# Kernel optimization log

Measured on AMD Instinct MI355X. Metric: run time of the kernel, lower is better.

## Reference

```python
import jax, jax.numpy as jnp
import numpy as np

ATTN_SIZE = 64
ENC_SIZE = 512
HIDDEN_SIZE = 512
L, B = 2048, 64


def setup_inputs() -> dict:
    key = jax.random.key(0)
    k1, k2, k3, k4, k5, k6 = jax.random.split(key, 6)
    enc_outputs = jax.random.normal(k1, (L, B, ENC_SIZE), dtype=jnp.float32)
    lens = jax.random.randint(k2, (B,), 1, L + 1, dtype=jnp.int32)
    hidden_states = jax.random.normal(k3, (B, HIDDEN_SIZE), dtype=jnp.float32)
    # Xavier-normal params as in reset_params()
    W_enc = jax.random.normal(k4, (ENC_SIZE, ATTN_SIZE), dtype=jnp.float32) * np.sqrt(2.0 / (ENC_SIZE + ATTN_SIZE))
    W_hidden = jax.random.normal(k5, (HIDDEN_SIZE, ATTN_SIZE), dtype=jnp.float32) * np.sqrt(2.0 / (HIDDEN_SIZE + ATTN_SIZE))
    b_attn = jnp.zeros((ATTN_SIZE,), dtype=jnp.float32)
    v = jax.random.normal(k6, (ATTN_SIZE,), dtype=jnp.float32)
    return {"enc_outputs": enc_outputs, "lens": lens, "hidden_states": hidden_states,
            "W_enc": W_enc, "b_attn": b_attn, "W_hidden": W_hidden, "v": v}


def reference(enc_outputs, lens, hidden_states, W_enc, b_attn, W_hidden, v):
    l = enc_outputs.shape[0]
    # parts: (l, b, attn_size) — projection of encoder outputs
    parts = jnp.einsum('lbd,da->lba', enc_outputs, W_enc) + b_attn
    # additive (Bahdanau) score: tanh(parts + h @ W_hidden) . v -> (l, b)
    hid = hidden_states @ W_hidden  # (b, attn_size)
    scores = jnp.sum(jnp.tanh(parts + hid[None, :, :]) * v, axis=2)
    # faithful mask: 1.0 at valid positions, -inf at padding (original adds 1, a
    # constant shift that softmax cancels, but we reproduce the exact math)
    valid = jnp.arange(l, dtype=lens.dtype)[:, None] < lens[None, :]  # (l, b)
    mask = jnp.where(valid, jnp.float32(1.0), -jnp.inf)
    w = jax.nn.softmax(scores + mask, axis=0)  # softmax over sequence dim
    # weighted sum over sequence: (b, d)
    return jnp.einsum('lb,lbd->bd', w, enc_outputs)
```

## Files before the change

kernel.cpp:

```cpp
#include <hip/hip_runtime.h>
#include <hip/hip_bf16.h>
#include <math.h>

#define L_DIM 2048
#define B_DIM 64
#define D_DIM 512
#define A_DIM 64

#define CHUNK_L 64
#define SUB_L 32
#define N_CHUNK (L_DIM / CHUNK_L)
#define EPAD 520

typedef __attribute__((ext_vector_type(8))) short bf16x8;
typedef __attribute__((ext_vector_type(4))) float f32x4;

__device__ __forceinline__ void split_bf16(float x, short& hi, short& lo) {
    __hip_bfloat16 h = __float2bfloat16(x);
    float hf = __bfloat162float(h);
    __hip_bfloat16 l = __float2bfloat16(x - hf);
    hi = *reinterpret_cast<short*>(&h);
    lo = *reinterpret_cast<short*>(&l);
}
__device__ __forceinline__ float bf16s_to_f(short s) {
    unsigned int u = ((unsigned int)(unsigned short)s) << 16;
    return __uint_as_float(u);
}

__global__ void hb_kernel(const float* __restrict__ hidden,
                          const float* __restrict__ Wh,
                          const float* __restrict__ battn,
                          float* __restrict__ hb) {
    const int b = blockIdx.x;
    const int a = threadIdx.x;
    const float* hrow = hidden + b * D_DIM;
    float acc = battn[a];
#pragma unroll 8
    for (int d = 0; d < D_DIM; ++d) acc += hrow[d] * Wh[d * A_DIM + a];
    hb[b * A_DIM + a] = acc;
}

__global__ __launch_bounds__(256) void wt_kernel(const float* __restrict__ We,
                                                 short* __restrict__ wt_hi,
                                                 short* __restrict__ wt_lo) {
    const int idx = blockIdx.x * 256 + threadIdx.x;
    const int a = idx & 63;
    const int d = idx >> 6;
    float x = We[d * A_DIM + a];
    short h, l;
    split_bf16(x, h, l);
    wt_hi[a * D_DIM + d] = h;
    wt_lo[a * D_DIM + d] = l;
}

__global__ __launch_bounds__(256) void fused_kernel(
    const float* __restrict__ enc, const short* __restrict__ wt_hi,
    const short* __restrict__ wt_lo, const float* __restrict__ hb,
    const float* __restrict__ v, const int* __restrict__ lens,
    float* __restrict__ Om, float* __restrict__ mz) {
    const int c = blockIdx.x;
    const int b = blockIdx.y;
    const int tid = threadIdx.x;
    const int wave = tid >> 6;
    const int lane = tid & 63;
    const int quad = lane >> 4;
    const int l15 = lane & 15;

    __shared__ short Ehi[SUB_L][EPAD];
    __shared__ short Elo[SUB_L][EPAD];
    __shared__ float sred[SUB_L][2];
    __shared__ float wl[SUB_L];
    __shared__ float red[4][D_DIM];
    __shared__ float msc[2];

    const int len_b = lens[b];

    const int lt = wave >> 1;
    const int ah = wave & 1;
    const int a0 = (2 * ah) * 16 + l15;
    const int a1 = a0 + 16;

    const float hb0 = hb[b * A_DIM + a0];
    const float hb1 = hb[b * A_DIM + a1];
    const float v0 = v[a0];
    const float v1 = v[a1];

    float Oacc[8];
#pragma unroll
    for (int i = 0; i < 8; ++i) Oacc[i] = 0.f;
    float mA = -INFINITY, ZA = 0.f;

    const int g = tid >> 6;
    const int d0 = (tid & 63) * 8;

#pragma unroll 1
    for (int sub = 0; sub < 2; ++sub) {
        const int l_base = c * CHUNK_L + sub * SUB_L;

        __syncthreads();

        {
            const float* src = enc + ((size_t)l_base * B_DIM + b) * D_DIM;
#pragma unroll
            for (int j = 0; j < 16; ++j) {
                const int idx = tid + 256 * j;
                const int li = idx >> 7;
                const int po = idx & 127;
                const float4 x =
                    *(const float4*)(src + (size_t)li * B_DIM * D_DIM + po * 4);
                short4 h4, l4;
                split_bf16(x.x, h4.x, l4.x);
                split_bf16(x.y, h4.y, l4.y);
                split_bf16(x.z, h4.z, l4.z);
                split_bf16(x.w, h4.w, l4.w);
                *(short4*)&Ehi[li][po * 4] = h4;
                *(short4*)&Elo[li][po * 4] = l4;
            }
        }
        __syncthreads();

        f32x4 acc0 = {0.f, 0.f, 0.f, 0.f};
        f32x4 acc1 = {0.f, 0.f, 0.f, 0.f};
        const short* brow0h = wt_hi + (size_t)a0 * D_DIM + quad * 8;
        const short* brow0l = wt_lo + (size_t)a0 * D_DIM + quad * 8;
        const short* brow1h = wt_hi + (size_t)a1 * D_DIM + quad * 8;
        const short* brow1l = wt_lo + (size_t)a1 * D_DIM + quad * 8;
        const int arow = lt * 16 + l15;
#pragma unroll 4
        for (int s = 0; s < 16; ++s) {
            const int k = s * 32;
            const bf16x8 Ah = *(const bf16x8*)&Ehi[arow][k + quad * 8];
            const bf16x8 Al = *(const bf16x8*)&Elo[arow][k + quad * 8];
            const bf16x8 B0h = *(const bf16x8*)(brow0h + k);
            const bf16x8 B0l = *(const bf16x8*)(brow0l + k);
            const bf16x8 B1h = *(const bf16x8*)(brow1h + k);
            const bf16x8 B1l = *(const bf16x8*)(brow1l + k);
            acc0 = __builtin_amdgcn_mfma_f32_16x16x32_bf16(Ah, B0h, acc0, 0, 0, 0);
            acc0 = __builtin_amdgcn_mfma_f32_16x16x32_bf16(Ah, B0l, acc0, 0, 0, 0);
            acc0 = __builtin_amdgcn_mfma_f32_16x16x32_bf16(Al, B0h, acc0, 0, 0, 0);
            acc1 = __builtin_amdgcn_mfma_f32_16x16x32_bf16(Ah, B1h, acc1, 0, 0, 0);
            acc1 = __builtin_amdgcn_mfma_f32_16x16x32_bf16(Ah, B1l, acc1, 0, 0, 0);
            acc1 = __builtin_amdgcn_mfma_f32_16x16x32_bf16(Al, B1h, acc1, 0, 0, 0);
        }

#pragma unroll
        for (int r = 0; r < 4; ++r) {
            float t = tanhf(acc0[r] + hb0) * v0 + tanhf(acc1[r] + hb1) * v1;
            t += __shfl_xor(t, 1);
            t += __shfl_xor(t, 2);
            t += __shfl_xor(t, 4);
            t += __shfl_xor(t, 8);
            if (l15 == 0) sred[lt * 16 + quad * 4 + r][ah] = t;
        }
        __syncthreads();

        if (tid < 32) {
            const int lg = l_base + tid;
            float s = sred[tid][0] + sred[tid][1];
            s = (lg < len_b) ? (s + 1.0f) : -INFINITY;
            float m = s;
            m = fmaxf(m, __shfl_xor(m, 1));
            m = fmaxf(m, __shfl_xor(m, 2));
            m = fmaxf(m, __shfl_xor(m, 4));
            m = fmaxf(m, __shfl_xor(m, 8));
            m = fmaxf(m, __shfl_xor(m, 16));
            const float w = (m == -INFINITY) ? 0.f : expf(s - m);
            wl[tid] = w;
            float z = w;
            z += __shfl_xor(z, 1);
            z += __shfl_xor(z, 2);
            z += __shfl_xor(z, 4);
            z += __shfl_xor(z, 8);
            z += __shfl_xor(z, 16);
            if (tid == 0) { msc[0] = m; msc[1] = z; }
        }
        __syncthreads();

        float pa[8];
#pragma unroll
        for (int i = 0; i < 8; ++i) pa[i] = 0.f;
#pragma unroll
        for (int li = 0; li < 8; ++li) {
            const int l = g * 8 + li;
            const float w = wl[l];
            const bf16x8 h8 = *(const bf16x8*)&Ehi[l][d0];
            const bf16x8 l8 = *(const bf16x8*)&Elo[l][d0];
#pragma unroll
            for (int i = 0; i < 8; ++i) {
                pa[i] += w * (bf16s_to_f(h8[i]) + bf16s_to_f(l8[i]));
            }
        }
        *(float4*)&red[g][d0] = make_float4(pa[0], pa[1], pa[2], pa[3]);
        *(float4*)&red[g][d0 + 4] = make_float4(pa[4], pa[5], pa[6], pa[7]);
        __syncthreads();

        const float m_sub = msc[0], Z_sub = msc[1];
        const float mN = fmaxf(mA, m_sub);
        const float cA = (mA == -INFINITY) ? 0.f : expf(mA - mN);
        const float cS = (m_sub == -INFINITY) ? 0.f : expf(m_sub - mN);
        if (tid < 64) {
            const int dd = tid * 8;
#pragma unroll
            for (int i = 0; i < 8; ++i) {
                const float os =
                    red[0][dd + i] + red[1][dd + i] + red[2][dd + i] + red[3][dd + i];
                Oacc[i] = cA * Oacc[i] + cS * os;
            }
        }
        ZA = cA * ZA + cS * Z_sub;
        mA = mN;
    }

    if (tid < 64) {
        float* dst = Om + ((size_t)b * N_CHUNK + c) * D_DIM + tid * 8;
        *(float4*)dst = make_float4(Oacc[0], Oacc[1], Oacc[2], Oacc[3]);
        *(float4*)(dst + 4) = make_float4(Oacc[4], Oacc[5], Oacc[6], Oacc[7]);
    }
    if (tid == 0) {
        mz[((size_t)b * N_CHUNK + c) * 2 + 0] = mA;
        mz[((size_t)b * N_CHUNK + c) * 2 + 1] = ZA;
    }
}

__global__ __launch_bounds__(256) void combine_kernel(
    const float* __restrict__ Om, const float* __restrict__ mz,
    float* __restrict__ out) {
    const int b = blockIdx.x;
    const int tid = threadIdx.x;
    __shared__ float coef[N_CHUNK];
    __shared__ float sinv;

    if (tid < 32) {
        const float m = mz[((size_t)b * N_CHUNK + tid) * 2 + 0];
        const float Z = mz[((size_t)b * N_CHUNK + tid) * 2 + 1];
        float mm = m;
        mm = fmaxf(mm, __shfl_xor(mm, 1));
        mm = fmaxf(mm, __shfl_xor(mm, 2));
        mm = fmaxf(mm, __shfl_xor(mm, 4));
        mm = fmaxf(mm, __shfl_xor(mm, 8));
        mm = fmaxf(mm, __shfl_xor(mm, 16));
        const float cc = (m == -INFINITY) ? 0.f : expf(m - mm);
        coef[tid] = cc;
        float s = cc * Z;
        s += __shfl_xor(s, 1);
        s += __shfl_xor(s, 2);
        s += __shfl_xor(s, 4);
        s += __shfl_xor(s, 8);
        s += __shfl_xor(s, 16);
        if (tid == 0) sinv = 1.0f / s;
    }
    __syncthreads();

    const float* base = Om + (size_t)b * N_CHUNK * D_DIM + tid * 2;
    float ox = 0.f, oy = 0.f;
#pragma unroll 8
    for (int cc = 0; cc < N_CHUNK; ++cc) {
        const float2 x = *(const float2*)(base + cc * D_DIM);
        ox += coef[cc] * x.x;
        oy += coef[cc] * x.y;
    }
    const float s = sinv;
    *(float2*)(out + (size_t)b * D_DIM + tid * 2) = make_float2(ox * s, oy * s);
}

__global__ __launch_bounds__(256) void scores_kernel(
    const float* __restrict__ enc, const float* __restrict__ We,
    const float* __restrict__ hb, const float* __restrict__ v,
    const int* __restrict__ lens, float* __restrict__ scores) {
    const int l = blockIdx.x;
    const int tid = threadIdx.x;
    const int ty = tid >> 4;
    const int tx = tid & 15;

    __shared__ float As[32][68];
    __shared__ float Bs[32][68];
    __shared__ float redl[64][17];

    float acc[4][4] = {};
    float4 areg[2], breg[2];
    const float* encl = enc + (size_t)l * B_DIM * D_DIM;

    auto loadTiles = [&](int k0) {
#pragma unroll
        for (int i = 0; i < 2; ++i) {
            const int cc = tid + 256 * i;
            const int bb = cc >> 3, kq = cc & 7;
            areg[i] = *(const float4*)(encl + bb * D_DIM + k0 + kq * 4);
            const int kk = cc >> 4, a4 = (cc & 15) * 4;
            breg[i] = *(const float4*)(We + (k0 + kk) * A_DIM + a4);
        }
    };
    auto storeTiles = [&]() {
#pragma unroll
        for (int i = 0; i < 2; ++i) {
            const int cc = tid + 256 * i;
            const int bb = cc >> 3, kq = cc & 7;
            As[kq * 4 + 0][bb] = areg[i].x;
            As[kq * 4 + 1][bb] = areg[i].y;
            As[kq * 4 + 2][bb] = areg[i].z;
            As[kq * 4 + 3][bb] = areg[i].w;
            const int kk = cc >> 4, a4 = (cc & 15) * 4;
            *(float4*)&Bs[kk][a4] = breg[i];
        }
    };

    loadTiles(0);
#pragma unroll 1
    for (int t = 0; t < 16; ++t) {
        __syncthreads();
        storeTiles();
        __syncthreads();
        if (t < 15) loadTiles((t + 1) * 32);
#pragma unroll
        for (int k = 0; k < 32; ++k) {
            const float4 av = *(const float4*)&As[k][ty * 4];
            const float4 bv = *(const float4*)&Bs[k][tx * 4];
            acc[0][0] += av.x * bv.x; acc[0][1] += av.x * bv.y;
            acc[0][2] += av.x * bv.z; acc[0][3] += av.x * bv.w;
            acc[1][0] += av.y * bv.x; acc[1][1] += av.y * bv.y;
            acc[1][2] += av.y * bv.z; acc[1][3] += av.y * bv.w;
            acc[2][0] += av.z * bv.x; acc[2][1] += av.z * bv.y;
            acc[2][2] += av.z * bv.z; acc[2][3] += av.z * bv.w;
            acc[3][0] += av.w * bv.x; acc[3][1] += av.w * bv.y;
            acc[3][2] += av.w * bv.z; acc[3][3] += av.w * bv.w;
        }
    }

    const float4 vv = *(const float4*)(v + tx * 4);
#pragma unroll
    for (int i = 0; i < 4; ++i) {
        const int bb = ty * 4 + i;
        const float4 hbv = *(const float4*)(hb + bb * A_DIM + tx * 4);
        float s = tanhf(acc[i][0] + hbv.x) * vv.x;
        s += tanhf(acc[i][1] + hbv.y) * vv.y;
        s += tanhf(acc[i][2] + hbv.z) * vv.z;
        s += tanhf(acc[i][3] + hbv.w) * vv.w;
        redl[bb][tx] = s;
    }
    __syncthreads();
    if (tid < B_DIM) {
        const int bb = tid;
        float s = 0.f;
#pragma unroll
        for (int j = 0; j < 16; ++j) s += redl[bb][j];
        s = (l < lens[bb]) ? (s + 1.0f) : -INFINITY;
        scores[(size_t)bb * L_DIM + l] = s;
    }
}

__global__ __launch_bounds__(256) void softmax_kernel(float* __restrict__ scores) {
    const int b = blockIdx.x;
    const int tid = threadIdx.x;
    float* s = scores + (size_t)b * L_DIM;
    __shared__ float red[256];

    float m = -INFINITY;
    for (int l = tid; l < L_DIM; l += 256) m = fmaxf(m, s[l]);
    red[tid] = m;
    __syncthreads();
    for (int off = 128; off > 0; off >>= 1) {
        if (tid < off) red[tid] = fmaxf(red[tid], red[tid + off]);
        __syncthreads();
    }
    m = red[0];
    __syncthreads();

    float z = 0.f;
    for (int l = tid; l < L_DIM; l += 256) z += expf(s[l] - m);
    red[tid] = z;
    __syncthreads();
    for (int off = 128; off > 0; off >>= 1) {
        if (tid < off) red[tid] += red[tid + off];
        __syncthreads();
    }
    const float inv = 1.0f / red[0];
    for (int l = tid; l < L_DIM; l += 256) s[l] = expf(s[l] - m) * inv;
}

__global__ __launch_bounds__(256) void zero_out_kernel(float* __restrict__ out) {
    out[blockIdx.x * 256 + threadIdx.x] = 0.f;
}

__global__ __launch_bounds__(128) void wsum_kernel(
    const float* __restrict__ enc, const float* __restrict__ w,
    float* __restrict__ out) {
    const int b = blockIdx.x;
    const int lc = blockIdx.y;
    const int tid = threadIdx.x;
    const int l0 = lc * (L_DIM / 16);

    float4 acc = {0.f, 0.f, 0.f, 0.f};
#pragma unroll 4
    for (int l = l0; l < l0 + (L_DIM / 16); ++l) {
        const float wt = w[(size_t)b * L_DIM + l];
        const float4 e =
            *(const float4*)(enc + ((size_t)l * B_DIM + b) * D_DIM + tid * 4);
        acc.x += wt * e.x; acc.y += wt * e.y;
        acc.z += wt * e.z; acc.w += wt * e.w;
    }
    float* o = out + (size_t)b * D_DIM + tid * 4;
    atomicAdd(o + 0, acc.x);
    atomicAdd(o + 1, acc.y);
    atomicAdd(o + 2, acc.z);
    atomicAdd(o + 3, acc.w);
}

extern "C" void kernel_launch(void* const* d_in, const int* in_sizes, int n_in,
                              void* d_out, int out_size, void* d_ws, size_t ws_size,
                              hipStream_t stream) {
    const float* enc    = (const float*)d_in[0];
    const int*   lens   = (const int*)d_in[1];
    const float* hidden = (const float*)d_in[2];
    const float* We     = (const float*)d_in[3];
    const float* battn  = (const float*)d_in[4];
    const float* Wh     = (const float*)d_in[5];
    const float* v      = (const float*)d_in[6];
    float* out = (float*)d_out;

    const size_t NEED = (size_t)160 * 1024 + (size_t)4 * 1024 * 1024;

    if (ws_size >= NEED) {
        char* w8 = (char*)d_ws;
        float* hb    = (float*)(w8 + 0);
        short* wt_hi = (short*)(w8 + 16 * 1024);
        short* wt_lo = (short*)(w8 + 80 * 1024);
        float* mz    = (float*)(w8 + 144 * 1024);
        float* Om    = (float*)(w8 + 160 * 1024);

        hb_kernel<<<B_DIM, A_DIM, 0, stream>>>(hidden, Wh, battn, hb);
        wt_kernel<<<(D_DIM * A_DIM) / 256, 256, 0, stream>>>(We, wt_hi, wt_lo);
        fused_kernel<<<dim3(N_CHUNK, B_DIM), 256, 0, stream>>>(
            enc, wt_hi, wt_lo, hb, v, lens, Om, mz);
        combine_kernel<<<B_DIM, 256, 0, stream>>>(Om, mz, out);
    } else {
        float* hb     = (float*)d_ws;
        float* scores = hb + B_DIM * A_DIM;

        hb_kernel<<<B_DIM, A_DIM, 0, stream>>>(hidden, Wh, battn, hb);
        scores_kernel<<<L_DIM, 256, 0, stream>>>(enc, We, hb, v, lens, scores);
        softmax_kernel<<<B_DIM, 256, 0, stream>>>(scores);
        zero_out_kernel<<<(B_DIM * D_DIM) / 256, 256, 0, stream>>>(out);
        wsum_kernel<<<dim3(B_DIM, 16), 128, 0, stream>>>(enc, scores, out);
    }
}
```

Measured before the change: 509.1 us.

## Register-prefetch encoder rows and accumulate weighted sum from registers in fused attention kernel

Restructures the fused kernel to process 16-row sub-chunks, with each thread holding its encoder float4s in registers. The next sub-chunk's rows are prefetched into registers while the MFMA score computation runs. The weighted sum is accumulated straight from the fp32 register copies instead of re-reading the bf16 hi/lo split from shared memory, removing a shared-memory reduction and a barrier per sub-chunk. It also deletes the fallback non-fused path, so the code now assumes the workspace is large enough. The cost is more registers (cur/nxt arrays) and smaller MFMA tiles with more sub-chunk iterations.

```diff
diff --git a/kernel.cpp b/kernel.cpp
--- a/kernel.cpp
+++ b/kernel.cpp
@@ -7,8 +7,9 @@
 #define D_DIM 512
 #define A_DIM 64
 
+#define SUB_L 16
 #define CHUNK_L 64
-#define SUB_L 32
+#define N_SUB (CHUNK_L / SUB_L)
 #define N_CHUNK (L_DIM / CHUNK_L)
 #define EPAD 520
 
@@ -22,9 +23,12 @@
     hi = *reinterpret_cast<short*>(&h);
     lo = *reinterpret_cast<short*>(&l);
 }
-__device__ __forceinline__ float bf16s_to_f(short s) {
-    unsigned int u = ((unsigned int)(unsigned short)s) << 16;
-    return __uint_as_float(u);
+
+__device__ __forceinline__ void split4(const float4& x, short4& h, short4& l) {
+    split_bf16(x.x, h.x, l.x);
+    split_bf16(x.y, h.y, l.y);
+    split_bf16(x.z, h.z, l.z);
+    split_bf16(x.w, h.w, l.w);
 }
 
 __global__ void hb_kernel(const float* __restrict__ hidden,
@@ -65,105 +69,88 @@
     const int lane = tid & 63;
     const int quad = lane >> 4;
     const int l15 = lane & 15;
+    const int po = tid & 127;
+    const int par = tid >> 7;
 
     __shared__ short Ehi[SUB_L][EPAD];
     __shared__ short Elo[SUB_L][EPAD];
-    __shared__ float sred[SUB_L][2];
+    __shared__ float sred[SUB_L][4];
     __shared__ float wl[SUB_L];
-    __shared__ float red[4][D_DIM];
     __shared__ float msc[2];
+    __shared__ float ored[D_DIM];
 
     const int len_b = lens[b];
-
-    const int lt = wave >> 1;
-    const int ah = wave & 1;
-    const int a0 = (2 * ah) * 16 + l15;
-    const int a1 = a0 + 16;
-
-    const float hb0 = hb[b * A_DIM + a0];
-    const float hb1 = hb[b * A_DIM + a1];
-    const float v0 = v[a0];
-    const float v1 = v[a1];
-
-    float Oacc[8];
-#pragma unroll
-    for (int i = 0; i < 8; ++i) Oacc[i] = 0.f;
+    const int a_col = wave * 16 + l15;
+    const float hb0 = hb[b * A_DIM + a_col];
+    const float v0 = v[a_col];
+
+    float4 Oacc = {0.f, 0.f, 0.f, 0.f};
     float mA = -INFINITY, ZA = 0.f;
 
-    const int g = tid >> 6;
-    const int d0 = (tid & 63) * 8;
+    const float* encb = enc + (size_t)c * CHUNK_L * B_DIM * D_DIM +
+                        (size_t)b * D_DIM + po * 4;
+    const size_t ROWSTRIDE = (size_t)B_DIM * D_DIM;
+
+    float4 cur[8], nxt[8];
+#pragma unroll
+    for (int j = 0; j < 8; ++j)
+        cur[j] = *(const float4*)(encb + (size_t)(2 * j + par) * ROWSTRIDE);
+
+    const short* bh = wt_hi + (size_t)a_col * D_DIM + quad * 8;
+    const short* bl = wt_lo + (size_t)a_col * D_DIM + quad * 8;
 
 #pragma unroll 1
-    for (int sub = 0; sub < 2; ++sub) {
-        const int l_base = c * CHUNK_L + sub * SUB_L;
-
+    for (int sub = 0; sub < N_SUB; ++sub) {
+#pragma unroll
+        for (int j = 0; j < 8; ++j) {
+            const int li = 2 * j + par;
+            short4 h4, l4;
+            split4(cur[j], h4, l4);
+            *(short4*)&Ehi[li][po * 4] = h4;
+            *(short4*)&Elo[li][po * 4] = l4;
+        }
         __syncthreads();
 
-        {
-            const float* src = enc + ((size_t)l_base * B_DIM + b) * D_DIM;
-#pragma unroll
-            for (int j = 0; j < 16; ++j) {
-                const int idx = tid + 256 * j;
-                const int li = idx >> 7;
-                const int po = idx & 127;
-                const float4 x =
-                    *(const float4*)(src + (size_t)li * B_DIM * D_DIM + po * 4);
-                short4 h4, l4;
-                split_bf16(x.x, h4.x, l4.x);
-                split_bf16(x.y, h4.y, l4.y);
-                split_bf16(x.z, h4.z, l4.z);
-                split_bf16(x.w, h4.w, l4.w);
-                *(short4*)&Ehi[li][po * 4] = h4;
-                *(short4*)&Elo[li][po * 4] = l4;
-            }
-        }
-        __syncthreads();
-
-        f32x4 acc0 = {0.f, 0.f, 0.f, 0.f};
-        f32x4 acc1 = {0.f, 0.f, 0.f, 0.f};
-        const short* brow0h = wt_hi + (size_t)a0 * D_DIM + quad * 8;
-        const short* brow0l = wt_lo + (size_t)a0 * D_DIM + quad * 8;
-        const short* brow1h = wt_hi + (size_t)a1 * D_DIM + quad * 8;
-        const short* brow1l = wt_lo + (size_t)a1 * D_DIM + quad * 8;
-        const int arow = lt * 16 + l15;
+        if (sub + 1 < N_SUB) {
+            const float* p = encb + (size_t)(sub + 1) * SUB_L * ROWSTRIDE;
+#pragma unroll
+            for (int j = 0; j < 8; ++j)
+                nxt[j] = *(const float4*)(p + (size_t)(2 * j + par) * ROWSTRIDE);
+        }
+
+        f32x4 acc = {0.f, 0.f, 0.f, 0.f};
 #pragma unroll 4
         for (int s = 0; s < 16; ++s) {
             const int k = s * 32;
-            const bf16x8 Ah = *(const bf16x8*)&Ehi[arow][k + quad * 8];
-            const bf16x8 Al = *(const bf16x8*)&Elo[arow][k + quad * 8];
-            const bf16x8 B0h = *(const bf16x8*)(brow0h + k);
-            const bf16x8 B0l = *(const bf16x8*)(brow0l + k);
-            const bf16x8 B1h = *(const bf16x8*)(brow1h + k);
-            const bf16x8 B1l = *(const bf16x8*)(brow1l + k);
-            acc0 = __builtin_amdgcn_mfma_f32_16x16x32_bf16(Ah, B0h, acc0, 0, 0, 0);
-            acc0 = __builtin_amdgcn_mfma_f32_16x16x32_bf16(Ah, B0l, acc0, 0, 0, 0);
-            acc0 = __builtin_amdgcn_mfma_f32_16x16x32_bf16(Al, B0h, acc0, 0, 0, 0);
-            acc1 = __builtin_amdgcn_mfma_f32_16x16x32_bf16(Ah, B1h, acc1, 0, 0, 0);
-            acc1 = __builtin_amdgcn_mfma_f32_16x16x32_bf16(Ah, B1l, acc1, 0, 0, 0);
-            acc1 = __builtin_amdgcn_mfma_f32_16x16x32_bf16(Al, B1h, acc1, 0, 0, 0);
+            const bf16x8 Ah = *(const bf16x8*)&Ehi[l15][k + quad * 8];
+            const bf16x8 Al = *(const bf16x8*)&Elo[l15][k + quad * 8];
+            const bf16x8 Bh = *(const bf16x8*)(bh + k);
+            const bf16x8 Bl = *(const bf16x8*)(bl + k);
+            acc = __builtin_amdgcn_mfma_f32_16x16x32_bf16(Ah, Bh, acc, 0, 0, 0);
+            acc = __builtin_amdgcn_mfma_f32_16x16x32_bf16(Ah, Bl, acc, 0, 0, 0);
+            acc = __builtin_amdgcn_mfma_f32_16x16x32_bf16(Al, Bh, acc, 0, 0, 0);
         }
 
 #pragma unroll
         for (int r = 0; r < 4; ++r) {
-            float t = tanhf(acc0[r] + hb0) * v0 + tanhf(acc1[r] + hb1) * v1;
+            float t = tanhf(acc[r] + hb0) * v0;
             t += __shfl_xor(t, 1);
             t += __shfl_xor(t, 2);
             t += __shfl_xor(t, 4);
             t += __shfl_xor(t, 8);
-            if (l15 == 0) sred[lt * 16 + quad * 4 + r][ah] = t;
+            if (l15 == 0) sred[quad * 4 + r][wave] = t;
         }
         __syncthreads();
 
-        if (tid < 32) {
-            const int lg = l_base + tid;
-            float s = sred[tid][0] + sred[tid][1];
+        if (tid < SUB_L) {
+            const int lg = c * CHUNK_L + sub * SUB_L + tid;
+            float s = sred[tid][0] + sred[tid][1] + sred[tid][2] + sred[tid][3];
             s = (lg < len_b) ? (s + 1.0f) : -INFINITY;
             float m = s;
             m = fmaxf(m, __shfl_xor(m, 1));
             m = fmaxf(m, __shfl_xor(m, 2));
             m = fmaxf(m, __shfl_xor(m, 4));
             m = fmaxf(m, __shfl_xor(m, 8));
-            m = fmaxf(m, __shfl_xor(m, 16));
             const float w = (m == -INFINITY) ? 0.f : expf(s - m);
             wl[tid] = w;
             float z = w;
@@ -171,50 +158,40 @@
             z += __shfl_xor(z, 2);
             z += __shfl_xor(z, 4);
             z += __shfl_xor(z, 8);
-            z += __shfl_xor(z, 16);
             if (tid == 0) { msc[0] = m; msc[1] = z; }
         }
-        __syncthreads();
-
-        float pa[8];
-#pragma unroll
-        for (int i = 0; i < 8; ++i) pa[i] = 0.f;
-#pragma unroll
-        for (int li = 0; li < 8; ++li) {
-            const int l = g * 8 + li;
-            const float w = wl[l];
-            const bf16x8 h8 = *(const bf16x8*)&Ehi[l][d0];
-            const bf16x8 l8 = *(const bf16x8*)&Elo[l][d0];
-#pragma unroll
-            for (int i = 0; i < 8; ++i) {
-                pa[i] += w * (bf16s_to_f(h8[i]) + bf16s_to_f(l8[i]));
-            }
-        }
-        *(float4*)&red[g][d0] = make_float4(pa[0], pa[1], pa[2], pa[3]);
-        *(float4*)&red[g][d0 + 4] = make_float4(pa[4], pa[5], pa[6], pa[7]);
         __syncthreads();
 
         const float m_sub = msc[0], Z_sub = msc[1];
         const float mN = fmaxf(mA, m_sub);
         const float cA = (mA == -INFINITY) ? 0.f : expf(mA - mN);
         const float cS = (m_sub == -INFINITY) ? 0.f : expf(m_sub - mN);
-        if (tid < 64) {
-            const int dd = tid * 8;
-#pragma unroll
-            for (int i = 0; i < 8; ++i) {
-                const float os =
-                    red[0][dd + i] + red[1][dd + i] + red[2][dd + i] + red[3][dd + i];
-                Oacc[i] = cA * Oacc[i] + cS * os;
-            }
+        Oacc.x *= cA; Oacc.y *= cA; Oacc.z *= cA; Oacc.w *= cA;
+#pragma unroll
+        for (int j = 0; j < 8; ++j) {
+            const float w = cS * wl[2 * j + par];
+            Oacc.x += w * cur[j].x;
+            Oacc.y += w * cur[j].y;
+            Oacc.z += w * cur[j].z;
+            Oacc.w += w * cur[j].w;
         }
         ZA = cA * ZA + cS * Z_sub;
         mA = mN;
-    }
-
-    if (tid < 64) {
-        float* dst = Om + ((size_t)b * N_CHUNK + c) * D_DIM + tid * 8;
-        *(float4*)dst = make_float4(Oacc[0], Oacc[1], Oacc[2], Oacc[3]);
-        *(float4*)(dst + 4) = make_float4(Oacc[4], Oacc[5], Oacc[6], Oacc[7]);
+
+#pragma unroll
+        for (int j = 0; j < 8; ++j) cur[j] = nxt[j];
+    }
+
+    if (par == 0) *(float4*)&ored[po * 4] = Oacc;
+    __syncthreads();
+    if (par == 1) {
+        const float4 o0 = *(const float4*)&ored[po * 4];
+        float4 r;
+        r.x = o0.x + Oacc.x;
+        r.y = o0.y + Oacc.y;
+        r.z = o0.z + Oacc.z;
+        r.w = o0.w + Oacc.w;
+        *(float4*)(Om + ((size_t)b * N_CHUNK + c) * D_DIM + po * 4) = r;
     }
     if (tid == 0) {
         mz[((size_t)b * N_CHUNK + c) * 2 + 0] = mA;
@@ -263,148 +240,6 @@
     *(float2*)(out + (size_t)b * D_DIM + tid * 2) = make_float2(ox * s, oy * s);
 }
 
-__global__ __launch_bounds__(256) void scores_kernel(
-    const float* __restrict__ enc, const float* __restrict__ We,
-    const float* __restrict__ hb, const float* __restrict__ v,
-    const int* __restrict__ lens, float* __restrict__ scores) {
-    const int l = blockIdx.x;
-    const int tid = threadIdx.x;
-    const int ty = tid >> 4;
-    const int tx = tid & 15;
-
-    __shared__ float As[32][68];
-    __shared__ float Bs[32][68];
-    __shared__ float redl[64][17];
-
-    float acc[4][4] = {};
-    float4 areg[2], breg[2];
-    const float* encl = enc + (size_t)l * B_DIM * D_DIM;
-
-    auto loadTiles = [&](int k0) {
-#pragma unroll
-        for (int i = 0; i < 2; ++i) {
-            const int cc = tid + 256 * i;
-            const int bb = cc >> 3, kq = cc & 7;
-            areg[i] = *(const float4*)(encl + bb * D_DIM + k0 + kq * 4);
-            const int kk = cc >> 4, a4 = (cc & 15) * 4;
-            breg[i] = *(const float4*)(We + (k0 + kk) * A_DIM + a4);
-        }
-    };
-    auto storeTiles = [&]() {
-#pragma unroll
-        for (int i = 0; i < 2; ++i) {
-            const int cc = tid + 256 * i;
-            const int bb = cc >> 3, kq = cc & 7;
-            As[kq * 4 + 0][bb] = areg[i].x;
-            As[kq * 4 + 1][bb] = areg[i].y;
-            As[kq * 4 + 2][bb] = areg[i].z;
-            As[kq * 4 + 3][bb] = areg[i].w;
-            const int kk = cc >> 4, a4 = (cc & 15) * 4;
-            *(float4*)&Bs[kk][a4] = breg[i];
-        }
-    };
-
-    loadTiles(0);
-#pragma unroll 1
-    for (int t = 0; t < 16; ++t) {
-        __syncthreads();
-        storeTiles();
-        __syncthreads();
-        if (t < 15) loadTiles((t + 1) * 32);
-#pragma unroll
-        for (int k = 0; k < 32; ++k) {
-            const float4 av = *(const float4*)&As[k][ty * 4];
-            const float4 bv = *(const float4*)&Bs[k][tx * 4];
-            acc[0][0] += av.x * bv.x; acc[0][1] += av.x * bv.y;
-            acc[0][2] += av.x * bv.z; acc[0][3] += av.x * bv.w;
-            acc[1][0] += av.y * bv.x; acc[1][1] += av.y * bv.y;
-            acc[1][2] += av.y * bv.z; acc[1][3] += av.y * bv.w;
-            acc[2][0] += av.z * bv.x; acc[2][1] += av.z * bv.y;
-            acc[2][2] += av.z * bv.z; acc[2][3] += av.z * bv.w;
-            acc[3][0] += av.w * bv.x; acc[3][1] += av.w * bv.y;
-            acc[3][2] += av.w * bv.z; acc[3][3] += av.w * bv.w;
-        }
-    }
-
-    const float4 vv = *(const float4*)(v + tx * 4);
-#pragma unroll
-    for (int i = 0; i < 4; ++i) {
-        const int bb = ty * 4 + i;
-        const float4 hbv = *(const float4*)(hb + bb * A_DIM + tx * 4);
-        float s = tanhf(acc[i][0] + hbv.x) * vv.x;
-        s += tanhf(acc[i][1] + hbv.y) * vv.y;
-        s += tanhf(acc[i][2] + hbv.z) * vv.z;
-        s += tanhf(acc[i][3] + hbv.w) * vv.w;
-        redl[bb][tx] = s;
-    }
-    __syncthreads();
-    if (tid < B_DIM) {
-        const int bb = tid;
-        float s = 0.f;
-#pragma unroll
-        for (int j = 0; j < 16; ++j) s += redl[bb][j];
-        s = (l < lens[bb]) ? (s + 1.0f) : -INFINITY;
-        scores[(size_t)bb * L_DIM + l] = s;
-    }
-}
-
-__global__ __launch_bounds__(256) void softmax_kernel(float* __restrict__ scores) {
-    const int b = blockIdx.x;
-    const int tid = threadIdx.x;
-    float* s = scores + (size_t)b * L_DIM;
-    __shared__ float red[256];
-
-    float m = -INFINITY;
-    for (int l = tid; l < L_DIM; l += 256) m = fmaxf(m, s[l]);
-    red[tid] = m;
-    __syncthreads();
-    for (int off = 128; off > 0; off >>= 1) {
-        if (tid < off) red[tid] = fmaxf(red[tid], red[tid + off]);
-        __syncthreads();
-    }
-    m = red[0];
-    __syncthreads();
-
-    float z = 0.f;
-    for (int l = tid; l < L_DIM; l += 256) z += expf(s[l] - m);
-    red[tid] = z;
-    __syncthreads();
-    for (int off = 128; off > 0; off >>= 1) {
-        if (tid < off) red[tid] += red[tid + off];
-        __syncthreads();
-    }
-    const float inv = 1.0f / red[0];
-    for (int l = tid; l < L_DIM; l += 256) s[l] = expf(s[l] - m) * inv;
-}
-
-__global__ __launch_bounds__(256) void zero_out_kernel(float* __restrict__ out) {
-    out[blockIdx.x * 256 + threadIdx.x] = 0.f;
-}
-
-__global__ __launch_bounds__(128) void wsum_kernel(
-    const float* __restrict__ enc, const float* __restrict__ w,
-    float* __restrict__ out) {
-    const int b = blockIdx.x;
-    const int lc = blockIdx.y;
-    const int tid = threadIdx.x;
-    const int l0 = lc * (L_DIM / 16);
-
-    float4 acc = {0.f, 0.f, 0.f, 0.f};
-#pragma unroll 4
-    for (int l = l0; l < l0 + (L_DIM / 16); ++l) {
-        const float wt = w[(size_t)b * L_DIM + l];
-        const float4 e =
-            *(const float4*)(enc + ((size_t)l * B_DIM + b) * D_DIM + tid * 4);
-        acc.x += wt * e.x; acc.y += wt * e.y;
-        acc.z += wt * e.z; acc.w += wt * e.w;
-    }
-    float* o = out + (size_t)b * D_DIM + tid * 4;
-    atomicAdd(o + 0, acc.x);
-    atomicAdd(o + 1, acc.y);
-    atomicAdd(o + 2, acc.z);
-    atomicAdd(o + 3, acc.w);
-}
-
 extern "C" void kernel_launch(void* const* d_in, const int* in_sizes, int n_in,
                               void* d_out, int out_size, void* d_ws, size_t ws_size,
                               hipStream_t stream) {
@@ -417,29 +252,16 @@
     const float* v      = (const float*)d_in[6];
     float* out = (float*)d_out;
 
-    const size_t NEED = (size_t)160 * 1024 + (size_t)4 * 1024 * 1024;
-
-    if (ws_size >= NEED) {
-        char* w8 = (char*)d_ws;
-        float* hb    = (float*)(w8 + 0);
-        short* wt_hi = (short*)(w8 + 16 * 1024);
-        short* wt_lo = (short*)(w8 + 80 * 1024);
-        float* mz    = (float*)(w8 + 144 * 1024);
-        float* Om    = (float*)(w8 + 160 * 1024);
-
-        hb_kernel<<<B_DIM, A_DIM, 0, stream>>>(hidden, Wh, battn, hb);
-        wt_kernel<<<(D_DIM * A_DIM) / 256, 256, 0, stream>>>(We, wt_hi, wt_lo);
-        fused_kernel<<<dim3(N_CHUNK, B_DIM), 256, 0, stream>>>(
-            enc, wt_hi, wt_lo, hb, v, lens, Om, mz);
-        combine_kernel<<<B_DIM, 256, 0, stream>>>(Om, mz, out);
-    } else {
-        float* hb     = (float*)d_ws;
-        float* scores = hb + B_DIM * A_DIM;
-
-        hb_kernel<<<B_DIM, A_DIM, 0, stream>>>(hidden, Wh, battn, hb);
-        scores_kernel<<<L_DIM, 256, 0, stream>>>(enc, We, hb, v, lens, scores);
-        softmax_kernel<<<B_DIM, 256, 0, stream>>>(scores);
-        zero_out_kernel<<<(B_DIM * D_DIM) / 256, 256, 0, stream>>>(out);
-        wsum_kernel<<<dim3(B_DIM, 16), 128, 0, stream>>>(enc, scores, out);
-    }
-}
+    char* w8 = (char*)d_ws;
+    float* hb    = (float*)(w8 + 0);
+    short* wt_hi = (short*)(w8 + 16 * 1024);
+    short* wt_lo = (short*)(w8 + 80 * 1024);
+    float* mz    = (float*)(w8 + 144 * 1024);
+    float* Om    = (float*)(w8 + 160 * 1024);
+
+    hb_kernel<<<B_DIM, A_DIM, 0, stream>>>(hidden, Wh, battn, hb);
+    wt_kernel<<<(D_DIM * A_DIM) / 256, 256, 0, stream>>>(We, wt_hi, wt_lo);
+    fused_kernel<<<dim3(N_CHUNK, B_DIM), 256, 0, stream>>>(
+        enc, wt_hi, wt_lo, hb, v, lens, Om, mz);
+    combine_kernel<<<B_DIM, 256, 0, stream>>>(Om, mz, out);
+}
```

Measured after the change: 498.1 us. -2.2%, faster.
